# Optimization experiments

Hardware: AMD Instinct MI355X
Metric: run time of the kernel (lower is better)

The kernel has to match this reference:

```python
import jax, jax.numpy as jnp
import numpy as np

N = 50000      # nodes per side
E = 800000     # edges per side
G = 1024       # graphs per batch
VOCAB = 100000
EMB, GH, EH, OUT = 128, 256, 256, 128
HID = GH + EH


def setup_inputs() -> dict:
    key = jax.random.key(0)
    ks = jax.random.split(key, 32)

    def xav(k, shape):
        lim = float(np.sqrt(6.0 / (shape[0] + shape[1])))
        return jax.random.uniform(k, shape, jnp.float32, -lim, lim)

    inp = {
        "x1": jax.random.randint(ks[0], (N,), 0, 11),
        "edge_index1": jax.random.randint(ks[1], (2, E), 0, N),
        "ent1": jax.random.randint(ks[2], (G,), 0, VOCAB),
        "batch1": jnp.sort(jax.random.randint(ks[3], (N,), 0, G)),
        "x2": jax.random.randint(ks[4], (N,), 0, 11),
        "edge_index2": jax.random.randint(ks[5], (2, E), 0, N),
        "ent2": jax.random.randint(ks[6], (G,), 0, VOCAB),
        "batch2": jnp.sort(jax.random.randint(ks[7], (N,), 0, G)),
        # shared GCN params (xavier weights, zero biases as in _reset_params)
        "atom_emb": xav(ks[8], (11, EMB)),
        "gW1": xav(ks[9], (EMB, GH)), "gb1": jnp.zeros((GH,), jnp.float32),
        "gW2": xav(ks[10], (GH, GH)), "gb2": jnp.zeros((GH,), jnp.float32),
        "fcW": xav(ks[11], (GH, GH)), "fcb": jnp.zeros((GH,), jnp.float32),
        # shared entity encoder params
        "ent_emb": xav(ks[12], (VOCAB, EMB)),
        "eW1": xav(ks[13], (EMB, EH)), "eb1": jnp.zeros((EH,), jnp.float32),
        "eW2": xav(ks[14], (EH, EH)), "eb2": jnp.zeros((EH,), jnp.float32),
        # decoder params
        "dW1": xav(ks[15], (HID, HID)), "db1": jnp.zeros((HID,), jnp.float32),
        "dW2": xav(ks[16], (HID, HID)), "db2": jnp.zeros((HID,), jnp.float32),
        "dW3": xav(ks[17], (HID, OUT)), "db3": jnp.zeros((OUT,), jnp.float32),
    }
    return inp


def _gcn_conv(x, W, b, src, dst, n):
    # PyG GCNConv: self-loops + symmetric normalization, out[dst] += norm * (x@W)[src]
    h = x @ W                                   # [n, d_out]
    loop = jnp.arange(n)
    s = jnp.concatenate([src, loop])
    d = jnp.concatenate([dst, loop])
    deg = jax.ops.segment_sum(jnp.ones_like(s, h.dtype), d, num_segments=n)
    dinv = jnp.where(deg > 0, jax.lax.rsqrt(jnp.maximum(deg, 1e-12)), 0.0)
    norm = dinv[s] * dinv[d]                    # [E+n]
    out = jax.ops.segment_sum(h[s] * norm[:, None], d, num_segments=n)
    return out + b


def _gcn_branch(x, edge_index, batch, atom_emb, gW1, gb1, gW2, gb2, fcW, fcb):
    src, dst = edge_index[0], edge_index[1]
    h = atom_emb[x]                             # [N, EMB]
    h = jax.nn.relu(_gcn_conv(h, gW1, gb1, src, dst, N))
    h = jax.nn.relu(_gcn_conv(h, gW2, gb2, src, dst, N))
    # global mean pool per graph
    counts = jax.ops.segment_sum(jnp.ones((N,), h.dtype), batch, num_segments=G)
    pooled = jax.ops.segment_sum(h, batch, num_segments=G) / jnp.maximum(counts, 1.0)[:, None]
    return pooled @ fcW + fcb                   # [G, GH]


def _enc(ent, ent_emb, eW1, eb1, eW2, eb2):
    e = jax.nn.relu(ent_emb[ent])
    e = jax.nn.relu(e @ eW1 + eb1)
    return jax.nn.relu(e @ eW2 + eb2)           # [G, EH]


def reference(x1, edge_index1, ent1, batch1, x2, edge_index2, ent2, batch2,
              atom_emb, gW1, gb1, gW2, gb2, fcW, fcb,
              ent_emb, eW1, eb1, eW2, eb2,
              dW1, db1, dW2, db2, dW3, db3):
    g1 = _gcn_branch(x1, edge_index1, batch1, atom_emb, gW1, gb1, gW2, gb2, fcW, fcb)
    g2 = _gcn_branch(x2, edge_index2, batch2, atom_emb, gW1, gb1, gW2, gb2, fcW, fcb)
    e1 = _enc(ent1, ent_emb, eW1, eb1, eW2, eb2)
    e2 = _enc(ent2, ent_emb, eW1, eb1, eW2, eb2)
    eg1 = jnp.concatenate([g1, e1], axis=1)     # [G, GH+EH]
    eg2 = jnp.concatenate([g2, e2], axis=1)
    egs = jax.nn.relu(eg1 + eg2)
    h = jax.nn.relu(egs @ dW1 + db1)
    h = jax.nn.relu(h @ dW2 + db2)
    return h @ dW3 + db3                        # [G, OUT]
```

## Files before the change

kernel.cpp:

```cpp
#include <hip/hip_runtime.h>
#include <hip/hip_fp16.h>

static constexpr int kN = 50000;
static constexpr int kE = 800000;
static constexpr int kG = 1024;
static constexpr int kEMB = 128;
static constexpr int kGH = 256;
static constexpr int kEH = 256;
static constexpr int kOUT = 128;
static constexpr int kHID = 512;
static constexpr int kNB = (kN + 255) / 256;
static constexpr int kMD = 64;
static constexpr int kNBKT = 196;
static constexpr int kEPB = 3125;
static constexpr int kPBLK = 256;

typedef __attribute__((ext_vector_type(8))) _Float16 half8v;
typedef __attribute__((ext_vector_type(4))) _Float16 half4v;
typedef __attribute__((ext_vector_type(4))) float floatx4;
typedef __attribute__((ext_vector_type(2))) float floatx2;


#define HS_SCALE 128.0f
#define HS_INV   (1.0f / 128.0f)

__device__ inline void acc_fp8x4(unsigned int w, float& a0, float& a1, float& a2, float& a3) {
    floatx2 lo = __builtin_amdgcn_cvt_pk_f32_fp8(w, false);
    floatx2 hi = __builtin_amdgcn_cvt_pk_f32_fp8(w, true);
    a0 += lo[0]; a1 += lo[1]; a2 += hi[0]; a3 += hi[1];
}

__device__ inline float grp16_reduce(float v) {
    int x;
    x = __builtin_amdgcn_update_dpp(0, __float_as_int(v), 0x121, 0xF, 0xF, true);
    v += __int_as_float(x);
    x = __builtin_amdgcn_update_dpp(0, __float_as_int(v), 0x122, 0xF, 0xF, true);
    v += __int_as_float(x);
    x = __builtin_amdgcn_update_dpp(0, __float_as_int(v), 0x124, 0xF, 0xF, true);
    v += __int_as_float(x);
    x = __builtin_amdgcn_update_dpp(0, __float_as_int(v), 0x128, 0xF, 0xF, true);
    v += __int_as_float(x);
    return v;
}

__global__ void prep_kernel(const float* __restrict__ atom_emb, const float* __restrict__ gW1,
                            const float* __restrict__ gW2,
                            float* __restrict__ M11, _Float16* __restrict__ w2t,
                            _Float16* __restrict__ m11t) {
    int i = blockIdx.x * 256 + threadIdx.x;
    if (blockIdx.x < 256) {
        int k = i >> 8, n = i & 255;
        w2t[(size_t)n * kGH + k] = (_Float16)gW2[(size_t)k * kGH + n];
    } else {
        int j = i - 65536;
        if (j < 11 * kGH) {
            int r = j >> 8, c = j & 255;
            float s = 0.f;
            for (int k = 0; k < kEMB; k++) s += atom_emb[r * kEMB + k] * gW1[k * kGH + c];
            M11[j] = s;
        } else if (j < 11 * kGH + 256 * 32) {
            int j2 = j - 11 * kGH;
            int n = j2 >> 5, k = j2 & 31;
            float s = 0.f;
            if (k < 11)
                for (int p = 0; p < kEMB; p++) s += atom_emb[k * kEMB + p] * gW1[p * kGH + n];
            m11t[j2] = (_Float16)s;
        }
    }
}

__global__ void wtrans_kernel(const float* __restrict__ dW1, const float* __restrict__ dW2,
                              const float* __restrict__ dW3, const float* __restrict__ fcW,
                              const float* __restrict__ eW1, const float* __restrict__ eW2,
                              _Float16* __restrict__ dW1t, _Float16* __restrict__ dW2t,
                              _Float16* __restrict__ dW3t, _Float16* __restrict__ fcWt,
                              _Float16* __restrict__ eW1t, _Float16* __restrict__ eW2t) {
    int b = blockIdx.x;
    const float* src; _Float16* dst; int K, N, j0;
    if (b < 1024)      { src = dW1; dst = dW1t; K = 512; N = 512; j0 = b * 256; }
    else if (b < 2048) { src = dW2; dst = dW2t; K = 512; N = 512; j0 = (b - 1024) * 256; }
    else if (b < 2304) { src = dW3; dst = dW3t; K = 512; N = 128; j0 = (b - 2048) * 256; }
    else if (b < 2560) { src = fcW; dst = fcWt; K = 256; N = 256; j0 = (b - 2304) * 256; }
    else if (b < 2688) { src = eW1; dst = eW1t; K = 128; N = 256; j0 = (b - 2560) * 256; }
    else               { src = eW2; dst = eW2t; K = 256; N = 256; j0 = (b - 2688) * 256; }
    int j = j0 + threadIdx.x;
    int n = j / K, k = j - n * K;
    dst[j] = (_Float16)src[(size_t)k * N + n];
}

__global__ void gbounds_kernel(const int* __restrict__ batch1, const int* __restrict__ batch2,
                               int* __restrict__ gstart) {
    int side = blockIdx.y;
    const int* batch = side ? batch2 : batch1;
    int g = blockIdx.x * 256 + threadIdx.x;
    if (g > kG) return;
    int lo = 0, hi = kN;
    while (lo < hi) { int mid = (lo + hi) >> 1; if (batch[mid] < g) lo = mid + 1; else hi = mid; }
    gstart[side * (kG + 1) + g] = lo;
}

__global__ void binp1_kernel(const int* __restrict__ ei1, const int* __restrict__ ei2,
                             int* __restrict__ poff) {
    int side = blockIdx.y;
    const int* dst = (side ? ei2 : ei1) + kE;
    __shared__ int hist[kNBKT];
    int t = threadIdx.x;
    if (t < kNBKT) hist[t] = 0;
    __syncthreads();
    int base = blockIdx.x * kEPB;
    for (int j = t; j < kEPB; j += 256)
        atomicAdd(&hist[dst[base + j] >> 8], 1);
    __syncthreads();
    if (t < kNBKT) poff[((side * kNBKT + t) << 8) | blockIdx.x] = hist[t];
}

__global__ void scanA_kernel(int* __restrict__ poff, int* __restrict__ btot) {
    int b = blockIdx.x, side = blockIdx.y, t = threadIdx.x;
    __shared__ int s[256];
    int idx = ((side * kNBKT + b) << 8) | t;
    int v = poff[idx];
    s[t] = v;
    __syncthreads();
    for (int o = 1; o < 256; o <<= 1) {
        int u = (t >= o) ? s[t - o] : 0;
        __syncthreads();
        s[t] += u;
        __syncthreads();
    }
    poff[idx] = s[t] - v;
    if (t == 255) btot[side * kNBKT + b] = s[255];
}

__global__ void scanB_kernel(const int* __restrict__ btot, int* __restrict__ bbase) {
    int side = blockIdx.x, t = threadIdx.x;
    __shared__ int s[256];
    int v = (t < kNBKT) ? btot[side * kNBKT + t] : 0;
    s[t] = v;
    __syncthreads();
    for (int o = 1; o < 256; o <<= 1) {
        int u = (t >= o) ? s[t - o] : 0;
        __syncthreads();
        s[t] += u;
        __syncthreads();
    }
    if (t < kNBKT) bbase[side * (kNBKT + 1) + t] = s[t] - v;
    if (t == 255) bbase[side * (kNBKT + 1) + kNBKT] = s[255];
}

__launch_bounds__(256)
__global__ void binp2_kernel(const int* __restrict__ ei1, const int* __restrict__ ei2,
                             const int* __restrict__ poff, const int* __restrict__ bbase,
                             unsigned int* __restrict__ ebuf) {
    int side = blockIdx.y, blk = blockIdx.x, t = threadIdx.x;
    const int* ei = side ? ei2 : ei1;
    __shared__ int hist[kNBKT], lb[kNBKT], gb[kNBKT], scanbuf[256];
    __shared__ unsigned int sorted[kEPB];
    if (t < kNBKT) hist[t] = 0;
    __syncthreads();
    int base = blk * kEPB;
    for (int j = t; j < kEPB; j += 256)
        atomicAdd(&hist[ei[kE + base + j] >> 8], 1);
    __syncthreads();
    int v = (t < kNBKT) ? hist[t] : 0;
    scanbuf[t] = v;
    __syncthreads();
    for (int o = 1; o < 256; o <<= 1) {
        int u = (t >= o) ? scanbuf[t - o] : 0;
        __syncthreads();
        scanbuf[t] += u;
        __syncthreads();
    }
    if (t < kNBKT) {
        lb[t] = scanbuf[t] - v;
        gb[t] = bbase[side * (kNBKT + 1) + t] + poff[((side * kNBKT + t) << 8) | blk];
        hist[t] = 0;
    }
    __syncthreads();
    for (int j = t; j < kEPB; j += 256) {
        int s_ = ei[base + j];
        int d  = ei[kE + base + j];
        int b  = d >> 8;
        int r  = atomicAdd(&hist[b], 1);
        sorted[lb[b] + r] = ((unsigned int)d << 16) | (unsigned int)s_;
    }
    __syncthreads();
    for (int j = t; j < kEPB; j += 256) {
        unsigned int val = sorted[j];
        int b = val >> 24;
        int gpos = gb[b] + (j - lb[b]);
        ebuf[(size_t)side * kE + gpos] = val;
    }
}

__global__ void binp3_kernel(const unsigned int* __restrict__ ebuf, const int* __restrict__ bbase,
                             unsigned short* __restrict__ col_ell, int* __restrict__ counts,
                             float* __restrict__ dinv, int2* __restrict__ xd,
                             const int* __restrict__ x1, const int* __restrict__ x2) {
    int b = blockIdx.x, side = blockIdx.y, t = threadIdx.x;
    __shared__ int cnt[256];
    cnt[t] = 0;
    __syncthreads();
    int start = bbase[side * (kNBKT + 1) + b];
    int end   = bbase[side * (kNBKT + 1) + b + 1];
    for (int k = start + t; k < end; k += 256) {
        unsigned int v = ebuf[(size_t)side * kE + k];
        int d8 = (v >> 16) & 255;
        int slot = atomicAdd(&cnt[d8], 1);
        if (slot > kMD - 1) slot = kMD - 1;
        int node = (b << 8) | d8;
        col_ell[((size_t)side * kN + node) * kMD + slot] = (unsigned short)(v & 0xFFFFu);
    }
    __syncthreads();
    int node = (b << 8) | t;
    if (node < kN) {
        int d = cnt[t];
        counts[side * kN + node] = d;
        float dv = rsqrtf((float)(d + 1));
        dinv[side * kN + node] = dv;
        const int* x = side ? x2 : x1;
        xd[side * kN + node] = make_int2(x[node], __float_as_int(dv));
    }
}

__global__ void conv1_wt_kernel(const int2* __restrict__ xd,
                                const int* __restrict__ counts,
                                const unsigned short* __restrict__ col_ell,
                                _Float16* __restrict__ wt16) {
    int side = blockIdx.y;
    const int2* xdb = xd + (size_t)side * kN;
    const int* deg = counts + side * kN;
    const unsigned short* ci = col_ell + (size_t)side * kN * kMD;
    _Float16* wb = wt16 + (size_t)side * kN * 32;

    int tid = threadIdx.x;
    int sub = tid & 15;
    int v = blockIdx.x * 16 + (tid >> 4);

    int cnt = min(deg[v], kMD);
    const unsigned short* cv = ci + (size_t)v * kMD;
    float wt[11];
    #pragma unroll
    for (int t = 0; t < 11; t++) wt[t] = 0.f;
    for (int base = 0; base < cnt; base += 16) {
        int e = base + sub;
        int xs = 15; float ds = 0.f;
        if (e < cnt) {
            int2 t = xdb[(int)cv[e]];
            xs = t.x; ds = __int_as_float(t.y);
        }
        #pragma unroll
        for (int t = 0; t < 11; t++) wt[t] += (xs == t) ? ds : 0.f;
    }
    #pragma unroll
    for (int t = 0; t < 11; t++) wt[t] = grp16_reduce(wt[t]);

    int2 xv = xdb[v];
    float dv = __int_as_float(xv.y);
    float dv2 = dv * dv;
    float mywt = 0.f;
    #pragma unroll
    for (int t = 0; t < 11; t++) mywt = (sub == t) ? wt[t] : mywt;
    float wp = dv * mywt + dv2 * ((xv.x == sub) ? 1.f : 0.f);
    wb[(size_t)v * 32 + sub] = (_Float16)wp;
    wb[(size_t)v * 32 + 16 + sub] = (_Float16)0.f;
}

__launch_bounds__(256)
__global__ void gemm2f_kernel(const _Float16* __restrict__ wt16,
                              const _Float16* __restrict__ m11t,
                              const float* __restrict__ b1,
                              const _Float16* __restrict__ Bt,
                              const float* __restrict__ dinv,
                              unsigned char* __restrict__ C) {
    __shared__ _Float16 As[128][72];
    __shared__ _Float16 Bs[128][72];

    int side = blockIdx.z;
    const _Float16* Aw = wt16 + (size_t)side * kN * 32;
    const float* db = dinv + (size_t)side * kN;
    unsigned char* Cb = C + (size_t)side * kN * kGH;

    int tid = threadIdx.x;
    int wave = tid >> 6, lane = tid & 63;
    int quad = lane >> 4, r = lane & 15;
    int wm = wave >> 1, wn = wave & 1;
    int row0 = blockIdx.x * 128;
    int col0 = blockIdx.y * 128;

    floatx4 acc[4][4];
    #pragma unroll
    for (int i = 0; i < 4; i++)
        #pragma unroll
        for (int j = 0; j < 4; j++) acc[i][j] = (floatx4){0.f, 0.f, 0.f, 0.f};

    half8v afw[2];
    #pragma unroll
    for (int mt = 0; mt < 2; mt++) {
        int gr = row0 + wave * 32 + mt * 16 + r;
        if (gr >= kN) gr = kN - 1;
        afw[mt] = *(const half8v*)(Aw + (size_t)gr * 32 + quad * 8);
    }

    for (int k0 = 0; k0 < kGH; k0 += 64) {
        #pragma unroll
        for (int u = 0; u < 4; u++) {
            int idx = tid + u * 256;
            int row = idx >> 3;
            int seg = (idx & 7) * 8;
            *(half8v*)&Bs[row][seg] = *(const half8v*)(Bt + (size_t)(col0 + row) * kGH + k0 + seg);
        }
        #pragma unroll
        for (int nt = 0; nt < 4; nt++) {
            half8v bfw = *(const half8v*)(m11t + (size_t)(k0 + nt * 16 + r) * 32 + quad * 8);
            float4 bia = *(const float4*)(b1 + k0 + nt * 16 + quad * 4);
            #pragma unroll
            for (int mt = 0; mt < 2; mt++) {
                floatx4 d = (floatx4){0.f, 0.f, 0.f, 0.f};
                d = __builtin_amdgcn_mfma_f32_16x16x32_f16(bfw, afw[mt], d, 0, 0, 0);
                half4v o;
                o[0] = (_Float16)fmaxf(d[0] + bia.x, 0.f);
                o[1] = (_Float16)fmaxf(d[1] + bia.y, 0.f);
                o[2] = (_Float16)fmaxf(d[2] + bia.z, 0.f);
                o[3] = (_Float16)fmaxf(d[3] + bia.w, 0.f);
                *(half4v*)&As[wave * 32 + mt * 16 + r][nt * 16 + quad * 4] = o;
            }
        }
        __syncthreads();
        #pragma unroll
        for (int ks = 0; ks < 2; ks++) {
            half8v af[4], bf[4];
            #pragma unroll
            for (int mt = 0; mt < 4; mt++)
                af[mt] = *(const half8v*)&As[wm * 64 + mt * 16 + r][ks * 32 + quad * 8];
            #pragma unroll
            for (int nt = 0; nt < 4; nt++)
                bf[nt] = *(const half8v*)&Bs[wn * 64 + nt * 16 + r][ks * 32 + quad * 8];
            #pragma unroll
            for (int mt = 0; mt < 4; mt++)
                #pragma unroll
                for (int nt = 0; nt < 4; nt++)
                    acc[mt][nt] = __builtin_amdgcn_mfma_f32_16x16x32_f16(af[mt], bf[nt],
                                                                         acc[mt][nt], 0, 0, 0);
        }
        __syncthreads();
    }

    #pragma unroll
    for (int mt = 0; mt < 4; mt++) {
        #pragma unroll
        for (int i = 0; i < 4; i++) {
            int grow = row0 + wm * 64 + mt * 16 + quad * 4 + i;
            if (grow >= kN) continue;
            float rsq = db[grow] * HS_SCALE;
            #pragma unroll
            for (int nt = 0; nt < 4; nt++) {
                int gcol = col0 + wn * 64 + nt * 16 + r;
                float q = acc[mt][nt][i] * rsq;
                Cb[(size_t)grow * kGH + gcol] =
                    (unsigned char)__builtin_amdgcn_cvt_pk_fp8_f32(q, q, 0, false);
            }
        }
    }
}

__launch_bounds__(256)
__global__ void gemm_tail_kernel(const _Float16* __restrict__ A,
                                 const _Float16* __restrict__ Bt,
                                 void* __restrict__ Cout,
                                 int N, int K,
                                 const float* __restrict__ bias,
                                 int relu, int f32out) {
    __shared__ _Float16 As[64][72];
    __shared__ _Float16 Bs[64][72];
    int tid = threadIdx.x;
    int wave = tid >> 6, lane = tid & 63;
    int quad = lane >> 4, r = lane & 15;
    int wm = wave >> 1, wn = wave & 1;
    int row0 = blockIdx.x * 64, col0 = blockIdx.y * 64;

    floatx4 acc[2][2];
    #pragma unroll
    for (int i = 0; i < 2; i++)
        #pragma unroll
        for (int j = 0; j < 2; j++) acc[i][j] = (floatx4){0.f, 0.f, 0.f, 0.f};

    for (int k0 = 0; k0 < K; k0 += 64) {
        #pragma unroll
        for (int u = 0; u < 2; u++) {
            int idx = tid + u * 256;
            int row = idx >> 3;
            int seg = (idx & 7) * 8;
            *(half8v*)&As[row][seg] = *(const half8v*)(A + (size_t)(row0 + row) * K + k0 + seg);
            *(half8v*)&Bs[row][seg] = *(const half8v*)(Bt + (size_t)(col0 + row) * K + k0 + seg);
        }
        __syncthreads();
        #pragma unroll
        for (int ks = 0; ks < 2; ks++) {
            half8v af[2], bf[2];
            #pragma unroll
            for (int mt = 0; mt < 2; mt++)
                af[mt] = *(const half8v*)&As[wm * 32 + mt * 16 + r][ks * 32 + quad * 8];
            #pragma unroll
            for (int nt = 0; nt < 2; nt++)
                bf[nt] = *(const half8v*)&Bs[wn * 32 + nt * 16 + r][ks * 32 + quad * 8];
            #pragma unroll
            for (int mt = 0; mt < 2; mt++)
                #pragma unroll
                for (int nt = 0; nt < 2; nt++)
                    acc[mt][nt] = __builtin_amdgcn_mfma_f32_16x16x32_f16(af[mt], bf[nt],
                                                                         acc[mt][nt], 0, 0, 0);
        }
        __syncthreads();
    }

    #pragma unroll
    for (int mt = 0; mt < 2; mt++) {
        #pragma unroll
        for (int i = 0; i < 4; i++) {
            int grow = row0 + wm * 32 + mt * 16 + quad * 4 + i;
            #pragma unroll
            for (int nt = 0; nt < 2; nt++) {
                int gcol = col0 + wn * 32 + nt * 16 + r;
                float v = acc[mt][nt][i] + bias[gcol];
                if (relu) v = fmaxf(v, 0.f);
                if (f32out) ((float*)Cout)[(size_t)grow * N + gcol] = v;
                else ((_Float16*)Cout)[(size_t)grow * N + gcol] = (_Float16)v;
            }
        }
    }
}

__global__ void aggregate2_kernel(const unsigned char* __restrict__ hs, const float* __restrict__ dinv,
                                  const int* __restrict__ counts,
                                  const unsigned short* __restrict__ col_ell,
                                  const float* __restrict__ bias, _Float16* __restrict__ out) {
    int side = blockIdx.y;
    const unsigned char* hb = hs + (size_t)side * kN * kGH;
    const float* dv_ = dinv + side * kN;
    const int* deg = counts + side * kN;
    const unsigned short* ci = col_ell + (size_t)side * kN * kMD;
    _Float16* ob = out + (size_t)side * kN * kGH;

    int wave = threadIdx.x >> 6;
    int lane = threadIdx.x & 63;
    int v = blockIdx.x * 4 + wave;
    if (v >= kN) return;
    int c = lane * 4;
    float4 bia = *(const float4*)(bias + c);
    float dv = dv_[v];
    float a0 = 0.f, a1 = 0.f, a2 = 0.f, a3 = 0.f;
    acc_fp8x4(*(const unsigned int*)(hb + (size_t)v * kGH + c), a0, a1, a2, a3);
    int cnt = min(deg[v], kMD);
    int idxl = (lane < cnt) ? (int)ci[(size_t)v * kMD + lane] : 0;
    int j = 0;
    for (; j + 16 <= cnt; j += 16) {
        unsigned int w[16];
        #pragma unroll
        for (int u = 0; u < 16; u++)
            w[u] = *(const unsigned int*)(hb + (size_t)__shfl(idxl, j + u) * kGH + c);
        #pragma unroll
        for (int u = 0; u < 16; u++) acc_fp8x4(w[u], a0, a1, a2, a3);
    }
    for (; j + 8 <= cnt; j += 8) {
        unsigned int w[8];
        #pragma unroll
        for (int u = 0; u < 8; u++)
            w[u] = *(const unsigned int*)(hb + (size_t)__shfl(idxl, j + u) * kGH + c);
        #pragma unroll
        for (int u = 0; u < 8; u++) acc_fp8x4(w[u], a0, a1, a2, a3);
    }
    for (; j < cnt; j++)
        acc_fp8x4(*(const unsigned int*)(hb + (size_t)__shfl(idxl, j) * kGH + c),
                  a0, a1, a2, a3);
    float f = dv * HS_INV;
    half4v o;
    o[0] = (_Float16)fmaxf(f * a0 + bia.x, 0.f);
    o[1] = (_Float16)fmaxf(f * a1 + bia.y, 0.f);
    o[2] = (_Float16)fmaxf(f * a2 + bia.z, 0.f);
    o[3] = (_Float16)fmaxf(f * a3 + bia.w, 0.f);
    __builtin_nontemporal_store(o, (half4v*)(ob + (size_t)v * kGH + c));
}

__global__ void poolfast_kernel(const _Float16* __restrict__ h,
                                const int* __restrict__ gstart,
                                _Float16* __restrict__ pooled16) {
    int side = blockIdx.y;
    int g = blockIdx.x;
    const _Float16* hb = h + (size_t)side * kN * kGH;
    int start = gstart[side * (kG + 1) + g];
    int end   = gstart[side * (kG + 1) + g + 1];
    int wave = threadIdx.x >> 6, lane = threadIdx.x & 63;
    int c = lane * 4;
    float a0 = 0.f, a1 = 0.f, a2 = 0.f, a3 = 0.f;
    for (int v = start + wave; v < end; v += 4) {
        half4v hv = *(const half4v*)(hb + (size_t)v * kGH + c);
        a0 += (float)hv[0]; a1 += (float)hv[1];
        a2 += (float)hv[2]; a3 += (float)hv[3];
    }
    __shared__ float ps[4][256];
    *(float4*)&ps[wave][c] = make_float4(a0, a1, a2, a3);
    __syncthreads();
    int t = threadIdx.x;
    float s = ps[0][t] + ps[1][t] + ps[2][t] + ps[3][t];
    float inv = 1.0f / fmaxf((float)(end - start), 1.0f);
    pooled16[(size_t)(side * kG + g) * kGH + t] = (_Float16)(s * inv);
}

__global__ void egather_kernel(const float* __restrict__ emb,
                               const int* __restrict__ ent1, const int* __restrict__ ent2,
                               _Float16* __restrict__ e16) {
    int rr = blockIdx.x;
    int idx = (rr < kG) ? ent1[rr] : ent2[rr - kG];
    int k = threadIdx.x;
    e16[(size_t)rr * kEMB + k] = (_Float16)fmaxf(emb[(size_t)idx * kEMB + k], 0.f);
}

__global__ void egsprep_kernel(const _Float16* __restrict__ gfc16,
                               const _Float16* __restrict__ ento16,
                               _Float16* __restrict__ egs16) {
    int idx = blockIdx.x * 256 + threadIdx.x;
    int g = idx >> 6;
    int k8 = (idx & 63) * 8;
    const _Float16* src = (k8 < kGH) ? gfc16 : ento16;
    int kk = (k8 < kGH) ? k8 : k8 - kGH;
    half8v a = *(const half8v*)(src + (size_t)g * kGH + kk);
    half8v b = *(const half8v*)(src + (size_t)(g + kG) * kGH + kk);
    half8v o;
    #pragma unroll
    for (int u = 0; u < 8; u++) o[u] = (_Float16)fmaxf((float)a[u] + (float)b[u], 0.f);
    *(half8v*)(egs16 + (size_t)g * kHID + k8) = o;
}

static inline char* carve(char*& p, size_t bytes) {
    char* r = p;
    p += (bytes + 255) & ~(size_t)255;
    return r;
}

extern "C" void kernel_launch(void* const* d_in, const int* in_sizes, int n_in,
                              void* d_out, int out_size, void* d_ws, size_t ws_size,
                              hipStream_t stream) {
    const int*   x1       = (const int*)d_in[0];
    const int*   ei1      = (const int*)d_in[1];
    const int*   ent1     = (const int*)d_in[2];
    const int*   batch1   = (const int*)d_in[3];
    const int*   x2       = (const int*)d_in[4];
    const int*   ei2      = (const int*)d_in[5];
    const int*   ent2     = (const int*)d_in[6];
    const int*   batch2   = (const int*)d_in[7];
    const float* atom_emb = (const float*)d_in[8];
    const float* gW1      = (const float*)d_in[9];
    const float* gb1      = (const float*)d_in[10];
    const float* gW2      = (const float*)d_in[11];
    const float* gb2      = (const float*)d_in[12];
    const float* fcW      = (const float*)d_in[13];
    const float* fcb      = (const float*)d_in[14];
    const float* ent_emb  = (const float*)d_in[15];
    const float* eW1      = (const float*)d_in[16];
    const float* eb1      = (const float*)d_in[17];
    const float* eW2      = (const float*)d_in[18];
    const float* eb2      = (const float*)d_in[19];
    const float* dW1      = (const float*)d_in[20];
    const float* db1      = (const float*)d_in[21];
    const float* dW2      = (const float*)d_in[22];
    const float* db2      = (const float*)d_in[23];
    const float* dW3      = (const float*)d_in[24];
    const float* db3      = (const float*)d_in[25];
    float* out = (float*)d_out;

    char* p = (char*)d_ws;
    _Float16* h4_h   = (_Float16*)carve(p, (size_t)2 * kN * kGH * 2);
    unsigned char* hs8 = (unsigned char*)carve(p, (size_t)2 * kN * kGH);
    unsigned short* col_ell = (unsigned short*)carve(p, (size_t)2 * kN * kMD * 2);
    unsigned int* ebuf = (unsigned int*)carve(p, (size_t)2 * kE * 4);
    int*   poff    = (int*)  carve(p, (size_t)2 * kNBKT * 256 * 4);
    int*   btot    = (int*)  carve(p, (size_t)2 * kNBKT * 4);
    int*   bbase   = (int*)  carve(p, (size_t)2 * (kNBKT + 1) * 4);
    int*   counts  = (int*)  carve(p, (size_t)2 * kN * 4);
    float* dinv    = (float*)carve(p, (size_t)2 * kN * 4);
    int2*  xd      = (int2*) carve(p, (size_t)2 * kN * 8);
    int*   gstart  = (int*)  carve(p, (size_t)2 * (kG + 1) * 4);
    float* M11     = (float*)carve(p, 11 * kGH * 4);
    _Float16* w2t  = (_Float16*)carve(p, (size_t)kGH * kGH * 2);
    _Float16* m11t = (_Float16*)carve(p, (size_t)256 * 32 * 2);
    _Float16* wt16 = (_Float16*)carve(p, (size_t)2 * kN * 32 * 2);
    _Float16* pooled16 = (_Float16*)carve(p, (size_t)2 * kG * kGH * 2);
    _Float16* gfc16    = (_Float16*)carve(p, (size_t)2 * kG * kGH * 2);
    _Float16* e16      = (_Float16*)carve(p, (size_t)2 * kG * kEMB * 2);
    _Float16* etmp16   = (_Float16*)carve(p, (size_t)2 * kG * kEH * 2);
    _Float16* ento16   = (_Float16*)carve(p, (size_t)2 * kG * kEH * 2);
    _Float16* egs16    = (_Float16*)carve(p, (size_t)kG * kHID * 2);
    _Float16* dh1_16   = (_Float16*)carve(p, (size_t)kG * kHID * 2);
    _Float16* dh2_16   = (_Float16*)carve(p, (size_t)kG * kHID * 2);
    _Float16* dW1t = (_Float16*)carve(p, (size_t)kHID * kHID * 2);
    _Float16* dW2t = (_Float16*)carve(p, (size_t)kHID * kHID * 2);
    _Float16* dW3t = (_Float16*)carve(p, (size_t)kOUT * kHID * 2);
    _Float16* fcWt = (_Float16*)carve(p, (size_t)kGH * kGH * 2);
    _Float16* eW1t = (_Float16*)carve(p, (size_t)kEH * kEMB * 2);
    _Float16* eW2t = (_Float16*)carve(p, (size_t)kEH * kEH * 2);

    prep_kernel<<<299, 256, 0, stream>>>(atom_emb, gW1, gW2, M11, w2t, m11t);
    wtrans_kernel<<<2944, 256, 0, stream>>>(dW1, dW2, dW3, fcW, eW1, eW2,
                                            dW1t, dW2t, dW3t, fcWt, eW1t, eW2t);
    gbounds_kernel<<<dim3((kG + 256) / 256, 2), 256, 0, stream>>>(batch1, batch2, gstart);
    binp1_kernel<<<dim3(kPBLK, 2), 256, 0, stream>>>(ei1, ei2, poff);
    scanA_kernel<<<dim3(kNBKT, 2), 256, 0, stream>>>(poff, btot);
    scanB_kernel<<<2, 256, 0, stream>>>(btot, bbase);
    binp2_kernel<<<dim3(kPBLK, 2), 256, 0, stream>>>(ei1, ei2, poff, bbase, ebuf);
    binp3_kernel<<<dim3(kNBKT, 2), 256, 0, stream>>>(ebuf, bbase, col_ell, counts,
                                                     dinv, xd, x1, x2);
    conv1_wt_kernel<<<dim3(kN / 16, 2), 256, 0, stream>>>(xd, counts, col_ell, wt16);
    gemm2f_kernel<<<dim3((kN + 127) / 128, kGH / 128, 2), 256, 0, stream>>>(
        wt16, m11t, gb1, w2t, dinv, hs8);
    aggregate2_kernel<<<dim3((kN + 3) / 4, 2), 256, 0, stream>>>(hs8, dinv, counts, col_ell,
                                                                 gb2, h4_h);
    poolfast_kernel<<<dim3(kG, 2), 256, 0, stream>>>(h4_h, gstart, pooled16);
    egather_kernel<<<2 * kG, 128, 0, stream>>>(ent_emb, ent1, ent2, e16);

    gemm_tail_kernel<<<dim3(2 * kG / 64, kGH / 64), 256, 0, stream>>>(
        pooled16, fcWt, gfc16, kGH, kGH, fcb, 0, 0);
    gemm_tail_kernel<<<dim3(2 * kG / 64, kEH / 64), 256, 0, stream>>>(
        e16, eW1t, etmp16, kEH, kEMB, eb1, 1, 0);
    gemm_tail_kernel<<<dim3(2 * kG / 64, kEH / 64), 256, 0, stream>>>(
        etmp16, eW2t, ento16, kEH, kEH, eb2, 1, 0);
    egsprep_kernel<<<kG * kHID / 8 / 256, 256, 0, stream>>>(gfc16, ento16, egs16);
    gemm_tail_kernel<<<dim3(kG / 64, kHID / 64), 256, 0, stream>>>(
        egs16, dW1t, dh1_16, kHID, kHID, db1, 1, 0);
    gemm_tail_kernel<<<dim3(kG / 64, kHID / 64), 256, 0, stream>>>(
        dh1_16, dW2t, dh2_16, kHID, kHID, db2, 1, 0);
    gemm_tail_kernel<<<dim3(kG / 64, kOUT / 64), 256, 0, stream>>>(
        dh2_16, dW3t, out, kOUT, kHID, db3, 0, 1);
}
```

Baseline: 395.1 us.

## Compute conv1 type weights from edge buckets and store layer-2 output as fp8

Replaces the per-node conv1 weight kernel, which gathered through the ELL column lists, with a bucket-based kernel. It streams the binned edge buffer and accumulates per-destination, per-atom-type weights with shared-memory atomics, then writes the fp16 weight rows with vector stores. Separately, the second aggregation now writes fp8 (scaled by 128) instead of fp16, and pooling reads fp8 and undoes the scale, which halves that intermediate's write and read traffic. The cost is extra quantization error in the pooled features, plus contention on shared-memory float atomics.

```diff
diff --git a/kernel.cpp b/kernel.cpp
--- a/kernel.cpp
+++ b/kernel.cpp
@@ -28,19 +28,6 @@
     floatx2 lo = __builtin_amdgcn_cvt_pk_f32_fp8(w, false);
     floatx2 hi = __builtin_amdgcn_cvt_pk_f32_fp8(w, true);
     a0 += lo[0]; a1 += lo[1]; a2 += hi[0]; a3 += hi[1];
-}
-
-__device__ inline float grp16_reduce(float v) {
-    int x;
-    x = __builtin_amdgcn_update_dpp(0, __float_as_int(v), 0x121, 0xF, 0xF, true);
-    v += __int_as_float(x);
-    x = __builtin_amdgcn_update_dpp(0, __float_as_int(v), 0x122, 0xF, 0xF, true);
-    v += __int_as_float(x);
-    x = __builtin_amdgcn_update_dpp(0, __float_as_int(v), 0x124, 0xF, 0xF, true);
-    v += __int_as_float(x);
-    x = __builtin_amdgcn_update_dpp(0, __float_as_int(v), 0x128, 0xF, 0xF, true);
-    v += __int_as_float(x);
-    return v;
 }
 
 __global__ void prep_kernel(const float* __restrict__ atom_emb, const float* __restrict__ gW1,
@@ -222,47 +209,42 @@
     }
 }
 
-__global__ void conv1_wt_kernel(const int2* __restrict__ xd,
-                                const int* __restrict__ counts,
-                                const unsigned short* __restrict__ col_ell,
-                                _Float16* __restrict__ wt16) {
-    int side = blockIdx.y;
+__global__ void binp4_kernel(const unsigned int* __restrict__ ebuf, const int* __restrict__ bbase,
+                             const int2* __restrict__ xd, _Float16* __restrict__ wt16) {
+    int b = blockIdx.x, side = blockIdx.y, t = threadIdx.x;
     const int2* xdb = xd + (size_t)side * kN;
-    const int* deg = counts + side * kN;
-    const unsigned short* ci = col_ell + (size_t)side * kN * kMD;
-    _Float16* wb = wt16 + (size_t)side * kN * 32;
-
-    int tid = threadIdx.x;
-    int sub = tid & 15;
-    int v = blockIdx.x * 16 + (tid >> 4);
-
-    int cnt = min(deg[v], kMD);
-    const unsigned short* cv = ci + (size_t)v * kMD;
-    float wt[11];
+    __shared__ float wtl[256][16];
     #pragma unroll
-    for (int t = 0; t < 11; t++) wt[t] = 0.f;
-    for (int base = 0; base < cnt; base += 16) {
-        int e = base + sub;
-        int xs = 15; float ds = 0.f;
-        if (e < cnt) {
-            int2 t = xdb[(int)cv[e]];
-            xs = t.x; ds = __int_as_float(t.y);
-        }
-        #pragma unroll
-        for (int t = 0; t < 11; t++) wt[t] += (xs == t) ? ds : 0.f;
-    }
-    #pragma unroll
-    for (int t = 0; t < 11; t++) wt[t] = grp16_reduce(wt[t]);
-
-    int2 xv = xdb[v];
-    float dv = __int_as_float(xv.y);
-    float dv2 = dv * dv;
-    float mywt = 0.f;
-    #pragma unroll
-    for (int t = 0; t < 11; t++) mywt = (sub == t) ? wt[t] : mywt;
-    float wp = dv * mywt + dv2 * ((xv.x == sub) ? 1.f : 0.f);
-    wb[(size_t)v * 32 + sub] = (_Float16)wp;
-    wb[(size_t)v * 32 + 16 + sub] = (_Float16)0.f;
+    for (int s = 0; s < 16; s++) wtl[t][s] = 0.f;
+    __syncthreads();
+    int start = bbase[side * (kNBKT + 1) + b];
+    int end   = bbase[side * (kNBKT + 1) + b + 1];
+    for (int k = start + t; k < end; k += 256) {
+        unsigned int v = ebuf[(size_t)side * kE + k];
+        int src = v & 0xFFFFu;
+        int d8 = (v >> 16) & 255;
+        int2 xs = xdb[src];
+        atomicAdd(&wtl[d8][xs.x], __int_as_float(xs.y));
+    }
+    __syncthreads();
+    int node = (b << 8) | t;
+    if (node < kN) {
+        int2 xv = xdb[node];
+        float dv = __int_as_float(xv.y);
+        float dv2 = dv * dv;
+        _Float16* wb = wt16 + ((size_t)side * kN + node) * 32;
+        half8v o0, o1, z;
+        #pragma unroll
+        for (int s = 0; s < 8; s++) {
+            o0[s] = (_Float16)(dv * wtl[t][s] + ((xv.x == s) ? dv2 : 0.f));
+            o1[s] = (_Float16)(dv * wtl[t][s + 8] + ((xv.x == s + 8) ? dv2 : 0.f));
+            z[s] = (_Float16)0.f;
+        }
+        *(half8v*)(wb) = o0;
+        *(half8v*)(wb + 8) = o1;
+        *(half8v*)(wb + 16) = z;
+        *(half8v*)(wb + 24) = z;
+    }
 }
 
 __launch_bounds__(256)
@@ -433,13 +415,13 @@
 __global__ void aggregate2_kernel(const unsigned char* __restrict__ hs, const float* __restrict__ dinv,
                                   const int* __restrict__ counts,
                                   const unsigned short* __restrict__ col_ell,
-                                  const float* __restrict__ bias, _Float16* __restrict__ out) {
+                                  const float* __restrict__ bias, unsigned char* __restrict__ out) {
     int side = blockIdx.y;
     const unsigned char* hb = hs + (size_t)side * kN * kGH;
     const float* dv_ = dinv + side * kN;
     const int* deg = counts + side * kN;
     const unsigned short* ci = col_ell + (size_t)side * kN * kMD;
-    _Float16* ob = out + (size_t)side * kN * kGH;
+    unsigned char* ob = out + (size_t)side * kN * kGH;
 
     int wave = threadIdx.x >> 6;
     int lane = threadIdx.x & 63;
@@ -473,36 +455,34 @@
         acc_fp8x4(*(const unsigned int*)(hb + (size_t)__shfl(idxl, j) * kGH + c),
                   a0, a1, a2, a3);
     float f = dv * HS_INV;
-    half4v o;
-    o[0] = (_Float16)fmaxf(f * a0 + bia.x, 0.f);
-    o[1] = (_Float16)fmaxf(f * a1 + bia.y, 0.f);
-    o[2] = (_Float16)fmaxf(f * a2 + bia.z, 0.f);
-    o[3] = (_Float16)fmaxf(f * a3 + bia.w, 0.f);
-    __builtin_nontemporal_store(o, (half4v*)(ob + (size_t)v * kGH + c));
-}
-
-__global__ void poolfast_kernel(const _Float16* __restrict__ h,
+    float q0 = fmaxf(f * a0 + bia.x, 0.f) * HS_SCALE;
+    float q1 = fmaxf(f * a1 + bia.y, 0.f) * HS_SCALE;
+    float q2 = fmaxf(f * a2 + bia.z, 0.f) * HS_SCALE;
+    float q3 = fmaxf(f * a3 + bia.w, 0.f) * HS_SCALE;
+    unsigned int w = __builtin_amdgcn_cvt_pk_fp8_f32(q0, q1, 0, false);
+    w = __builtin_amdgcn_cvt_pk_fp8_f32(q2, q3, w, true);
+    __builtin_nontemporal_store(w, (unsigned int*)(ob + (size_t)v * kGH + c));
+}
+
+__global__ void poolfast_kernel(const unsigned char* __restrict__ h,
                                 const int* __restrict__ gstart,
                                 _Float16* __restrict__ pooled16) {
     int side = blockIdx.y;
     int g = blockIdx.x;
-    const _Float16* hb = h + (size_t)side * kN * kGH;
+    const unsigned char* hb = h + (size_t)side * kN * kGH;
     int start = gstart[side * (kG + 1) + g];
     int end   = gstart[side * (kG + 1) + g + 1];
     int wave = threadIdx.x >> 6, lane = threadIdx.x & 63;
     int c = lane * 4;
     float a0 = 0.f, a1 = 0.f, a2 = 0.f, a3 = 0.f;
-    for (int v = start + wave; v < end; v += 4) {
-        half4v hv = *(const half4v*)(hb + (size_t)v * kGH + c);
-        a0 += (float)hv[0]; a1 += (float)hv[1];
-        a2 += (float)hv[2]; a3 += (float)hv[3];
-    }
+    for (int v = start + wave; v < end; v += 4)
+        acc_fp8x4(*(const unsigned int*)(hb + (size_t)v * kGH + c), a0, a1, a2, a3);
     __shared__ float ps[4][256];
     *(float4*)&ps[wave][c] = make_float4(a0, a1, a2, a3);
     __syncthreads();
     int t = threadIdx.x;
     float s = ps[0][t] + ps[1][t] + ps[2][t] + ps[3][t];
-    float inv = 1.0f / fmaxf((float)(end - start), 1.0f);
+    float inv = HS_INV / fmaxf((float)(end - start), 1.0f);
     pooled16[(size_t)(side * kG + g) * kGH + t] = (_Float16)(s * inv);
 }
 
@@ -569,8 +549,8 @@
     float* out = (float*)d_out;
 
     char* p = (char*)d_ws;
-    _Float16* h4_h   = (_Float16*)carve(p, (size_t)2 * kN * kGH * 2);
-    unsigned char* hs8 = (unsigned char*)carve(p, (size_t)2 * kN * kGH);
+    unsigned char* h4_8 = (unsigned char*)carve(p, (size_t)2 * kN * kGH);
+    unsigned char* hs8  = (unsigned char*)carve(p, (size_t)2 * kN * kGH);
     unsigned short* col_ell = (unsigned short*)carve(p, (size_t)2 * kN * kMD * 2);
     unsigned int* ebuf = (unsigned int*)carve(p, (size_t)2 * kE * 4);
     int*   poff    = (int*)  carve(p, (size_t)2 * kNBKT * 256 * 4);
@@ -609,12 +589,12 @@
     binp2_kernel<<<dim3(kPBLK, 2), 256, 0, stream>>>(ei1, ei2, poff, bbase, ebuf);
     binp3_kernel<<<dim3(kNBKT, 2), 256, 0, stream>>>(ebuf, bbase, col_ell, counts,
                                                      dinv, xd, x1, x2);
-    conv1_wt_kernel<<<dim3(kN / 16, 2), 256, 0, stream>>>(xd, counts, col_ell, wt16);
+    binp4_kernel<<<dim3(kNBKT, 2), 256, 0, stream>>>(ebuf, bbase, xd, wt16);
     gemm2f_kernel<<<dim3((kN + 127) / 128, kGH / 128, 2), 256, 0, stream>>>(
         wt16, m11t, gb1, w2t, dinv, hs8);
     aggregate2_kernel<<<dim3((kN + 3) / 4, 2), 256, 0, stream>>>(hs8, dinv, counts, col_ell,
-                                                                 gb2, h4_h);
-    poolfast_kernel<<<dim3(kG, 2), 256, 0, stream>>>(h4_h, gstart, pooled16);
+                                                                 gb2, h4_8);
+    poolfast_kernel<<<dim3(kG, 2), 256, 0, stream>>>(h4_8, gstart, pooled16);
     egather_kernel<<<2 * kG, 128, 0, stream>>>(ent_emb, ent1, ent2, e16);
 
     gemm_tail_kernel<<<dim3(2 * kG / 64, kGH / 64), 256, 0, stream>>>(
```

New measurement: 387.7 us. No clear change (-1.9%).
